# Kernel tuning notes

Hardware: AMD Instinct MI355X
Metric: run time of the kernel (lower is better)

Reference implementation:

```python
import jax, jax.numpy as jnp
import numpy as np

B, S, EMBED, HEADS = 2, 2048, 2048, 16
HEAD_DIM = EMBED // HEADS  # 128


def setup_inputs() -> dict:
    key = jax.random.key(0)
    k1, k2, k3 = jax.random.split(key, 3)
    x = jax.random.normal(k1, (B, S, EMBED), dtype=jnp.float32)
    # qkv_proj: Linear(EMBED -> 3*EMBED, bias=False); stored as [in, out]
    w_qkv = jax.random.normal(k2, (EMBED, 3 * EMBED), dtype=jnp.float32) / np.float32(np.sqrt(EMBED))
    # out_proj: Linear(EMBED -> EMBED, bias=False)
    w_out = jax.random.normal(k3, (EMBED, EMBED), dtype=jnp.float32) / np.float32(np.sqrt(EMBED))
    return {"x": x, "w_qkv": w_qkv, "w_out": w_out}


def reference(x, w_qkv, w_out):
    b, s, e = x.shape
    h, d = HEADS, e // HEADS
    qkv = x @ w_qkv                                  # [b, s, 3e]
    q, k, v = jnp.split(qkv, 3, axis=-1)             # each [b, s, e]
    q = q.reshape(b, s, h, d).transpose(0, 2, 1, 3)  # [b, h, s, d]
    k = k.reshape(b, s, h, d).transpose(0, 2, 1, 3)
    v = v.reshape(b, s, h, d).transpose(0, 2, 1, 3)
    scale = jnp.asarray(1.0 / np.sqrt(d), dtype=q.dtype)
    scores = jnp.einsum('bhqd,bhkd->bhqk', q, k) * scale  # [b, h, s, s]
    causal = jnp.tril(jnp.ones((s, s), dtype=bool))
    scores = jnp.where(causal, scores, -jnp.inf)
    attn = jax.nn.softmax(scores, axis=-1)
    ctx = jnp.einsum('bhqk,bhkd->bhqd', attn, v)     # [b, h, s, d]
    ctx = ctx.transpose(0, 2, 1, 3).reshape(b, s, e)
    return ctx @ w_out
```

## Files before the change

kernel.cpp:

```cpp
#include <hip/hip_runtime.h>
#include <cstdint>

#define S_LEN 2048
#define EMB   2048
#define NHEAD 16
#define HDIM  128
#define MROWS 4096
#define NQKV  6144

typedef __bf16 bf16x8 __attribute__((ext_vector_type(8)));
typedef __bf16 bf16x4 __attribute__((ext_vector_type(4)));
typedef float  f32x4  __attribute__((ext_vector_type(4)));

#define MFMA16(a, b, c) __builtin_amdgcn_mfma_f32_16x16x32_bf16((a), (b), (c), 0, 0, 0)

__device__ __forceinline__ unsigned short f2bf(float f) {
  unsigned u = __builtin_bit_cast(unsigned, f);
  u += 0x7fffu + ((u >> 16) & 1u);
  return (unsigned short)(u >> 16);
}
__device__ __forceinline__ float bf2f(unsigned short u) {
  unsigned v = ((unsigned)u) << 16;
  return __builtin_bit_cast(float, v);
}

__device__ __forceinline__ void gl_lds16(const unsigned short* g, unsigned short* l) {
  __builtin_amdgcn_global_load_lds(
      (const __attribute__((address_space(1))) void*)(uintptr_t)g,
      (__attribute__((address_space(3))) void*)(unsigned int)(uintptr_t)l,
      16, 0, 0);
}

__global__ void cast_bf16(const float* __restrict__ in, unsigned short* __restrict__ out, int n) {
  int i = (blockIdx.x * 256 + threadIdx.x) * 4;
  if (i >= n) return;
  float4 v = *(const float4*)(in + i);
  ushort4 o;
  o.x = f2bf(v.x); o.y = f2bf(v.y); o.z = f2bf(v.z); o.w = f2bf(v.w);
  *(ushort4*)(out + i) = o;
}

__global__ void transpose_cast(const float* __restrict__ in, unsigned short* __restrict__ out,
                               int R, int C) {
  __shared__ float tile[32][33];
  int bx = blockIdx.x << 5;
  int by = blockIdx.y << 5;
  int tx = threadIdx.x, ty = threadIdx.y;
  for (int j = 0; j < 32; j += 8)
    tile[ty + j][tx] = in[(size_t)(by + ty + j) * C + bx + tx];
  __syncthreads();
  for (int j = 0; j < 32; j += 8)
    out[(size_t)(bx + ty + j) * R + by + tx] = f2bf(tile[tx][ty + j]);
}

__global__ __launch_bounds__(256, 3) void gemm_qkv(const unsigned short* __restrict__ A,
                                                   const unsigned short* __restrict__ Bt,
                                                   unsigned short* __restrict__ Qo,
                                                   unsigned short* __restrict__ Ko,
                                                   unsigned short* __restrict__ Vt) {
  __shared__ __align__(16) unsigned short As[128 * 64];
  __shared__ __align__(16) unsigned short Bs[128 * 64];
  const int tid = threadIdx.x;
  const int n0 = blockIdx.x << 7;
  const int m0 = blockIdx.y << 7;
  const int wave = tid >> 6, lane = tid & 63;
  const int wm = (wave & 1) << 6, wn = (wave >> 1) << 6;
  const int fr = lane & 15, g = lane >> 4;
  const int q = tid >> 3;
  const int jp = tid & 7;
  f32x4 acc[4][4] = {};
  for (int k0 = 0; k0 < 2048; k0 += 64) {
    for (int i = 0; i < 4; ++i) {
      const int row = q + (i << 5);
      const int jsw = (jp ^ (row & 7)) << 3;
      gl_lds16(A + (size_t)(m0 + row) * 2048 + k0 + jsw, As + (row << 6) + (jp << 3));
      gl_lds16(Bt + (size_t)(n0 + row) * 2048 + k0 + jsw, Bs + (row << 6) + (jp << 3));
    }
    __builtin_amdgcn_s_waitcnt(0);
    __syncthreads();
    for (int ks = 0; ks < 2; ++ks) {
      const int slot = (((ks << 2) + g) ^ (fr & 7)) << 3;
      bf16x8 af[4], bfv[4];
      for (int i = 0; i < 4; ++i) af[i]  = *(const bf16x8*)(As + ((wm + (i << 4) + fr) << 6) + slot);
      for (int j = 0; j < 4; ++j) bfv[j] = *(const bf16x8*)(Bs + ((wn + (j << 4) + fr) << 6) + slot);
      for (int i = 0; i < 4; ++i)
        for (int j = 0; j < 4; ++j)
          acc[i][j] = MFMA16(af[i], bfv[j], acc[i][j]);
    }
    __syncthreads();
  }
  const int which = n0 >> 11;
  const int h = (n0 >> 7) & 15;
  const int bb = m0 >> 11;
  const int bh = bb * NHEAD + h;
  for (int i = 0; i < 4; ++i) {
    const int sl = (m0 & (S_LEN - 1)) + wm + (i << 4) + (g << 2);
    for (int j = 0; j < 4; ++j) {
      const int d = wn + (j << 4) + fr;
      if (which == 2) {
        ushort4 pk;
        pk.x = f2bf(acc[i][j][0]); pk.y = f2bf(acc[i][j][1]);
        pk.z = f2bf(acc[i][j][2]); pk.w = f2bf(acc[i][j][3]);
        *(ushort4*)(Vt + ((size_t)bh * HDIM + d) * S_LEN + sl) = pk;
      } else {
        unsigned short* dst = (which == 0) ? Qo : Ko;
        for (int r = 0; r < 4; ++r)
          dst[((size_t)bh * S_LEN + sl + r) * HDIM + d] = f2bf(acc[i][j][r]);
      }
    }
  }
}

__global__ __launch_bounds__(256, 3) void attn(const unsigned short* __restrict__ Qg,
                                               const unsigned short* __restrict__ Kg,
                                               const unsigned short* __restrict__ Vtg,
                                               unsigned short* __restrict__ ctx,
                                               unsigned short* __restrict__ Opart,
                                               float* __restrict__ Lp) {
  __shared__ __align__(16) unsigned short SA[16384];
  __shared__ __align__(16) unsigned short Ps[8192];
  unsigned short* Qs = SA;
  unsigned short* Ks = SA;
  unsigned short* Vs = SA + 8192;

  const int blk = blockIdx.x;
  const int bh = blk & 31;
  const int t = blk >> 5;
  int qt, kt0, nkt, part;
  if (t < 8)       { qt = t;     kt0 = 0;  nkt = 2 * t + 2;       part = -1; }
  else if (t < 16) { qt = t;     kt0 = 0;  nkt = 16;              part = (bh << 3) + (qt - 8); }
  else             { qt = t - 8; kt0 = 16; nkt = 2 * qt - 14;     part = 256 + (bh << 3) + (qt - 8); }

  const int tid = threadIdx.x, wave = tid >> 6, lane = tid & 63;
  const int fr = lane & 15, g = lane >> 4;

  const unsigned short* qsrc = Qg + ((size_t)bh * S_LEN + (qt << 7)) * HDIM;
  for (int i = 0; i < 8; ++i) {
    int s0 = (i * 256 + tid) << 3;
    int q = s0 >> 7, jp = (s0 >> 3) & 15;
    gl_lds16(qsrc + (q << 7) + ((jp ^ (q & 15)) << 3), Qs + s0);
  }
  __builtin_amdgcn_s_waitcnt(0);
  __syncthreads();

  bf16x8 qf[2][4];
  for (int nbq = 0; nbq < 2; ++nbq)
    for (int kd = 0; kd < 4; ++kd) {
      int q = (wave << 5) + (nbq << 4) + fr;
      qf[nbq][kd] = *(const bf16x8*)(Qs + (q << 7) + ((((kd << 2) + g) ^ fr) << 3));
    }
  __syncthreads();

  float lsum[2] = {0.f, 0.f};
  f32x4 oacc[2][8] = {};
  const float scale = 0.08838834764831845f;

  const unsigned short* kbase = Kg + (size_t)bh * S_LEN * HDIM;
  const unsigned short* vbase = Vtg + (size_t)bh * HDIM * S_LEN;

  for (int kti = 0; kti < nkt; ++kti) {
    const int kt = kt0 + kti;
    const unsigned short* ks = kbase + ((size_t)kt << 6) * HDIM;
    const unsigned short* vs = vbase + (kt << 6);
    for (int i = 0; i < 4; ++i) {
      int s0 = (i * 256 + tid) << 3;
      int key = s0 >> 7, jk = (s0 >> 3) & 15;
      gl_lds16(ks + (key << 7) + ((jk ^ (key & 15)) << 3), Ks + s0);
      int d = s0 >> 6, jv = (s0 >> 3) & 7;
      gl_lds16(vs + (size_t)d * S_LEN + ((jv ^ (d & 7)) << 3), Vs + s0);
    }
    __builtin_amdgcn_s_waitcnt(0);
    __syncthreads();

    f32x4 sacc[2][4] = {};
    for (int kd = 0; kd < 4; ++kd)
      for (int kb = 0; kb < 4; ++kb) {
        bf16x8 kf = *(const bf16x8*)(Ks + (((kb << 4) + fr) << 7) + ((((kd << 2) + g) ^ fr) << 3));
        sacc[0][kb] = MFMA16(kf, qf[0][kd], sacc[0][kb]);
        sacc[1][kb] = MFMA16(kf, qf[1][kd], sacc[1][kb]);
      }

    const bool diag = (kt >= 2 * qt);
    for (int nbq = 0; nbq < 2; ++nbq) {
      const int qg = (qt << 7) + (wave << 5) + (nbq << 4) + fr;
      float sum = 0.f;
      for (int kb = 0; kb < 4; ++kb) {
        float p[4];
        for (int r = 0; r < 4; ++r) {
          float v = sacc[nbq][kb][r] * scale;
          if (diag) {
            int keyg = (kt << 6) + (kb << 4) + (g << 2) + r;
            if (keyg > qg) v = -__builtin_inff();
          }
          p[r] = __expf(v);
          sum += p[r];
        }
        ushort4 pk;
        pk.x = f2bf(p[0]); pk.y = f2bf(p[1]); pk.z = f2bf(p[2]); pk.w = f2bf(p[3]);
        *(ushort4*)(Ps + (((wave << 3) + (nbq << 2) + kb) << 8) + (lane << 2)) = pk;
      }
      lsum[nbq] += sum;
    }

    __builtin_amdgcn_s_waitcnt(0);

    for (int kc = 0; kc < 2; ++kc) {
      const int kbr = (kc << 1) + (g >> 1);
      bf16x8 ap[2];
      for (int h2 = 0; h2 < 2; ++h2) {
        const unsigned short* pb =
            Ps + (((wave << 3) + (h2 << 2) + kbr) << 8) + ((g & 1) << 7) + (fr << 2);
        bf16x4 a0 = *(const bf16x4*)pb;
        bf16x4 a1 = *(const bf16x4*)(pb + 64);
        bf16x8 a;
        a[0] = a0[0]; a[1] = a0[1]; a[2] = a0[2]; a[3] = a0[3];
        a[4] = a1[0]; a[5] = a1[1]; a[6] = a1[2]; a[7] = a1[3];
        ap[h2] = a;
      }
      for (int nd = 0; nd < 8; ++nd) {
        bf16x8 bv = *(const bf16x8*)(Vs + (((nd << 4) + fr) << 6) + ((((kc << 2) + g) ^ (fr & 7)) << 3));
        oacc[0][nd] = MFMA16(ap[0], bv, oacc[0][nd]);
        oacc[1][nd] = MFMA16(ap[1], bv, oacc[1][nd]);
      }
    }
    __syncthreads();
  }

  for (int nbq = 0; nbq < 2; ++nbq) {
    lsum[nbq] += __shfl_xor(lsum[nbq], 16);
    lsum[nbq] += __shfl_xor(lsum[nbq], 32);
  }

  if (part < 0) {
    const int b = bh >> 4, h = bh & 15;
    for (int mq = 0; mq < 2; ++mq)
      for (int r = 0; r < 4; ++r) {
        float lv = __shfl(lsum[mq], (lane & 48) | ((g << 2) + r));
        const float il = 1.0f / lv;
        const int s = (qt << 7) + (wave << 5) + (mq << 4) + (g << 2) + r;
        unsigned short* dst = ctx + ((size_t)(b * S_LEN + s) * EMB) + (h << 7);
        for (int nd = 0; nd < 8; ++nd)
          dst[(nd << 4) + fr] = f2bf(oacc[mq][nd][r] * il);
      }
  } else {
    unsigned short* Ob = Opart + ((size_t)part << 14);
    for (int mq = 0; mq < 2; ++mq)
      for (int r = 0; r < 4; ++r) {
        const int ql = (wave << 5) + (mq << 4) + (g << 2) + r;
        unsigned short* dst = Ob + (ql << 7);
        for (int nd = 0; nd < 8; ++nd)
          dst[(nd << 4) + fr] = f2bf(oacc[mq][nd][r]);
      }
    if (g == 0)
      for (int nbq = 0; nbq < 2; ++nbq) {
        const int ql = (wave << 5) + (nbq << 4) + fr;
        Lp[(part << 7) + ql] = lsum[nbq];
      }
  }
}

__global__ void attn_combine(const unsigned short* __restrict__ Op,
                             const float* __restrict__ Lp,
                             unsigned short* __restrict__ ctx) {
  const int tid = threadIdx.x;
  const int rid = blockIdx.x * 16 + (tid >> 4);
  const int l16 = tid & 15;
  const int bh = rid >> 10;
  const int qtl = (rid >> 7) & 7;
  const int ql = rid & 127;
  const int p = (bh << 3) + qtl;
  const float lA = Lp[(p << 7) + ql];
  const float lB = Lp[((256 + p) << 7) + ql];
  const float il = 1.0f / (lA + lB);
  const int d0 = l16 << 3;
  const unsigned short* a = Op + ((size_t)p << 14) + (ql << 7) + d0;
  const unsigned short* b = Op + ((size_t)(256 + p) << 14) + (ql << 7) + d0;
  const int bb = bh >> 4, h = bh & 15;
  const int s = ((qtl + 8) << 7) + ql;
  unsigned short* dst = ctx + ((size_t)(bb * S_LEN + s) * EMB) + (h << 7) + d0;
  ushort4 va0 = *(const ushort4*)a, va1 = *(const ushort4*)(a + 4);
  ushort4 vb0 = *(const ushort4*)b, vb1 = *(const ushort4*)(b + 4);
  ushort4 o0, o1;
  o0.x = f2bf((bf2f(va0.x) + bf2f(vb0.x)) * il);
  o0.y = f2bf((bf2f(va0.y) + bf2f(vb0.y)) * il);
  o0.z = f2bf((bf2f(va0.z) + bf2f(vb0.z)) * il);
  o0.w = f2bf((bf2f(va0.w) + bf2f(vb0.w)) * il);
  o1.x = f2bf((bf2f(va1.x) + bf2f(vb1.x)) * il);
  o1.y = f2bf((bf2f(va1.y) + bf2f(vb1.y)) * il);
  o1.z = f2bf((bf2f(va1.z) + bf2f(vb1.z)) * il);
  o1.w = f2bf((bf2f(va1.w) + bf2f(vb1.w)) * il);
  *(ushort4*)dst = o0;
  *(ushort4*)(dst + 4) = o1;
}

__global__ __launch_bounds__(256, 3) void gemm_out(const unsigned short* __restrict__ A,
                                                   const unsigned short* __restrict__ Bt,
                                                   float* __restrict__ C) {
  __shared__ __align__(16) unsigned short As[128 * 64];
  __shared__ __align__(16) unsigned short Bs[128 * 64];
  const int tid = threadIdx.x;
  const int n0 = blockIdx.x << 7;
  const int m0 = blockIdx.y << 7;
  const int wave = tid >> 6, lane = tid & 63;
  const int wm = (wave & 1) << 6, wn = (wave >> 1) << 6;
  const int fr = lane & 15, g = lane >> 4;
  const int q = tid >> 3;
  const int jp = tid & 7;
  f32x4 acc[4][4] = {};
  for (int k0 = 0; k0 < 2048; k0 += 64) {
    for (int i = 0; i < 4; ++i) {
      const int row = q + (i << 5);
      const int jsw = (jp ^ (row & 7)) << 3;
      gl_lds16(A + (size_t)(m0 + row) * 2048 + k0 + jsw, As + (row << 6) + (jp << 3));
      gl_lds16(Bt + (size_t)(n0 + row) * 2048 + k0 + jsw, Bs + (row << 6) + (jp << 3));
    }
    __builtin_amdgcn_s_waitcnt(0);
    __syncthreads();
    for (int ks = 0; ks < 2; ++ks) {
      const int slot = (((ks << 2) + g) ^ (fr & 7)) << 3;
      bf16x8 af[4], bfv[4];
      for (int i = 0; i < 4; ++i) af[i]  = *(const bf16x8*)(As + ((wm + (i << 4) + fr) << 6) + slot);
      for (int j = 0; j < 4; ++j) bfv[j] = *(const bf16x8*)(Bs + ((wn + (j << 4) + fr) << 6) + slot);
      for (int i = 0; i < 4; ++i)
        for (int j = 0; j < 4; ++j)
          acc[i][j] = MFMA16(af[i], bfv[j], acc[i][j]);
    }
    __syncthreads();
  }
  for (int i = 0; i < 4; ++i) {
    const int row = m0 + wm + (i << 4) + (g << 2);
    for (int j = 0; j < 4; ++j) {
      const int col = n0 + wn + (j << 4) + fr;
      for (int r = 0; r < 4; ++r)
        C[(size_t)(row + r) * EMB + col] = acc[i][j][r];
    }
  }
}

extern "C" void kernel_launch(void* const* d_in, const int* in_sizes, int n_in,
                              void* d_out, int out_size, void* d_ws, size_t ws_size,
                              hipStream_t stream) {
  const float* x    = (const float*)d_in[0];
  const float* wqkv = (const float*)d_in[1];
  const float* wout = (const float*)d_in[2];
  float* out = (float*)d_out;

  unsigned short* ws = (unsigned short*)d_ws;
  const size_t NELEM = (size_t)MROWS * EMB;
  unsigned short* xb    = ws;
  unsigned short* wqkvT = xb + NELEM;
  unsigned short* woutT = wqkvT + (size_t)NQKV * EMB;
  unsigned short* Q     = woutT + (size_t)EMB * EMB;
  unsigned short* K     = Q + NELEM;
  unsigned short* Vt    = K + NELEM;
  unsigned short* ctx   = xb;
  unsigned short* Opart = wqkvT;
  float* Lp = (float*)(Opart + ((size_t)512 << 14));

  cast_bf16<<<8192, 256, 0, stream>>>(x, xb, (int)NELEM);
  transpose_cast<<<dim3(NQKV / 32, EMB / 32), dim3(32, 8), 0, stream>>>(wqkv, wqkvT, EMB, NQKV);
  transpose_cast<<<dim3(EMB / 32, EMB / 32), dim3(32, 8), 0, stream>>>(wout, woutT, EMB, EMB);
  gemm_qkv<<<dim3(NQKV / 128, MROWS / 128), 256, 0, stream>>>(xb, wqkvT, Q, K, Vt);
  attn<<<768, 256, 0, stream>>>(Q, K, Vt, ctx, Opart, Lp);
  attn_combine<<<2048, 256, 0, stream>>>(Opart, Lp, ctx);
  gemm_out<<<dim3(EMB / 128, MROWS / 128), 256, 0, stream>>>(ctx, woutT, out);
}
```

Baseline: 364.6 us.

## Replace QKV and output GEMMs with double-buffered 256x128-tile 8-wave pipeline

Both projection GEMMs now share a pipelined mainloop: 512-thread blocks compute 256x128 tiles and keep two K-stage buffers in dynamic LDS. The next stage's global-to-LDS loads are issued before the current stage's MFMAs, with a partial vmcnt wait so memory latency overlaps compute. The loop also splits the B fragment loads into two halves, raises wave priority around the MFMA bursts, and uses an XCD-aware block-index swizzle. The cost is 96KB of LDS per block, which limits occupancy to one block per CU, plus extra barriers per K step.

```diff
diff --git a/kernel.cpp b/kernel.cpp
--- a/kernel.cpp
+++ b/kernel.cpp
@@ -53,42 +53,115 @@
     out[(size_t)(bx + ty + j) * R + by + tx] = f2bf(tile[tx][ty + j]);
 }
 
-__global__ __launch_bounds__(256, 3) void gemm_qkv(const unsigned short* __restrict__ A,
-                                                   const unsigned short* __restrict__ Bt,
-                                                   unsigned short* __restrict__ Qo,
-                                                   unsigned short* __restrict__ Ko,
-                                                   unsigned short* __restrict__ Vt) {
-  __shared__ __align__(16) unsigned short As[128 * 64];
-  __shared__ __align__(16) unsigned short Bs[128 * 64];
+__device__ __forceinline__ void gemm_pipe(const unsigned short* __restrict__ Ap,
+                                          const unsigned short* __restrict__ Bp,
+                                          int m0, int n0, f32x4 (&acc)[4][4]) {
+  extern __shared__ unsigned short lds[];
+  unsigned short* As = lds;
+  unsigned short* Bs = lds + 32768;
   const int tid = threadIdx.x;
-  const int n0 = blockIdx.x << 7;
-  const int m0 = blockIdx.y << 7;
-  const int wave = tid >> 6, lane = tid & 63;
-  const int wm = (wave & 1) << 6, wn = (wave >> 1) << 6;
+  const int w = tid >> 6, lane = tid & 63;
   const int fr = lane & 15, g = lane >> 4;
-  const int q = tid >> 3;
-  const int jp = tid & 7;
+  const int wm = (w >> 1) << 6;
+  const int wn = (w & 1) << 6;
+  const int q = tid >> 3, jp = tid & 7;
+
+  auto stageA = [&](int buf, int kk) {
+#pragma unroll
+    for (int i = 0; i < 4; ++i) {
+      const int row = q + (i << 6);
+      gl_lds16(Ap + (size_t)(m0 + row) * 2048 + kk + ((jp ^ (row & 7)) << 3),
+               As + buf * 16384 + (row << 6) + (jp << 3));
+    }
+  };
+  auto stageB = [&](int buf, int kk) {
+#pragma unroll
+    for (int i = 0; i < 2; ++i) {
+      const int row = q + (i << 6);
+      gl_lds16(Bp + (size_t)(n0 + row) * 2048 + kk + ((jp ^ (row & 7)) << 3),
+               Bs + buf * 8192 + (row << 6) + (jp << 3));
+    }
+  };
+
+  stageA(0, 0); stageB(0, 0);
+  int cur = 0;
+#pragma unroll 2
+  for (int t = 0; t < 32; ++t) {
+    if (t < 31) {
+      const int kn = (t + 1) << 6;
+      stageA(cur ^ 1, kn); stageB(cur ^ 1, kn);
+      asm volatile("s_waitcnt vmcnt(6)" ::: "memory");
+    } else {
+      asm volatile("s_waitcnt vmcnt(0)" ::: "memory");
+    }
+    __builtin_amdgcn_s_barrier();
+    asm volatile("" ::: "memory");
+
+    const unsigned short* Ab = As + cur * 16384;
+    const unsigned short* Bb = Bs + cur * 8192;
+
+    bf16x8 af[4][2], bv[2][2];
+#pragma unroll
+    for (int i = 0; i < 4; ++i)
+#pragma unroll
+      for (int ks = 0; ks < 2; ++ks)
+        af[i][ks] = *(const bf16x8*)(Ab + ((wm + (i << 4) + fr) << 6) +
+                                     ((((ks << 2) + g) ^ (fr & 7)) << 3));
+#pragma unroll
+    for (int j = 0; j < 2; ++j)
+#pragma unroll
+      for (int ks = 0; ks < 2; ++ks)
+        bv[j][ks] = *(const bf16x8*)(Bb + ((wn + (j << 4) + fr) << 6) +
+                                     ((((ks << 2) + g) ^ (fr & 7)) << 3));
+    __builtin_amdgcn_s_setprio(1);
+#pragma unroll
+    for (int ks = 0; ks < 2; ++ks)
+#pragma unroll
+      for (int i = 0; i < 4; ++i)
+#pragma unroll
+        for (int j = 0; j < 2; ++j)
+          acc[i][j] = MFMA16(af[i][ks], bv[j][ks], acc[i][j]);
+    __builtin_amdgcn_s_setprio(0);
+    asm volatile("" ::: "memory");
+    __builtin_amdgcn_s_barrier();
+
+    bf16x8 bw[2][2];
+#pragma unroll
+    for (int j = 0; j < 2; ++j)
+#pragma unroll
+      for (int ks = 0; ks < 2; ++ks)
+        bw[j][ks] = *(const bf16x8*)(Bb + ((wn + ((j + 2) << 4) + fr) << 6) +
+                                     ((((ks << 2) + g) ^ (fr & 7)) << 3));
+    __builtin_amdgcn_s_setprio(1);
+#pragma unroll
+    for (int ks = 0; ks < 2; ++ks)
+#pragma unroll
+      for (int i = 0; i < 4; ++i)
+#pragma unroll
+        for (int j = 0; j < 2; ++j)
+          acc[i][j + 2] = MFMA16(af[i][ks], bw[j][ks], acc[i][j + 2]);
+    __builtin_amdgcn_s_setprio(0);
+    asm volatile("" ::: "memory");
+    __builtin_amdgcn_s_barrier();
+    cur ^= 1;
+  }
+}
+
+__global__ __launch_bounds__(512, 2) void gemm8_qkv(const unsigned short* __restrict__ A,
+                                                    const unsigned short* __restrict__ Bt,
+                                                    unsigned short* __restrict__ Qo,
+                                                    unsigned short* __restrict__ Ko,
+                                                    unsigned short* __restrict__ Vt) {
+  const int bid = blockIdx.x;
+  const int wg = (bid & 7) * 96 + (bid >> 3);
+  const int mt = wg / 48, nt = wg - mt * 48;
+  const int m0 = mt << 8, n0 = nt << 7;
   f32x4 acc[4][4] = {};
-  for (int k0 = 0; k0 < 2048; k0 += 64) {
-    for (int i = 0; i < 4; ++i) {
-      const int row = q + (i << 5);
-      const int jsw = (jp ^ (row & 7)) << 3;
-      gl_lds16(A + (size_t)(m0 + row) * 2048 + k0 + jsw, As + (row << 6) + (jp << 3));
-      gl_lds16(Bt + (size_t)(n0 + row) * 2048 + k0 + jsw, Bs + (row << 6) + (jp << 3));
-    }
-    __builtin_amdgcn_s_waitcnt(0);
-    __syncthreads();
-    for (int ks = 0; ks < 2; ++ks) {
-      const int slot = (((ks << 2) + g) ^ (fr & 7)) << 3;
-      bf16x8 af[4], bfv[4];
-      for (int i = 0; i < 4; ++i) af[i]  = *(const bf16x8*)(As + ((wm + (i << 4) + fr) << 6) + slot);
-      for (int j = 0; j < 4; ++j) bfv[j] = *(const bf16x8*)(Bs + ((wn + (j << 4) + fr) << 6) + slot);
-      for (int i = 0; i < 4; ++i)
-        for (int j = 0; j < 4; ++j)
-          acc[i][j] = MFMA16(af[i], bfv[j], acc[i][j]);
-    }
-    __syncthreads();
-  }
+  gemm_pipe(A, Bt, m0, n0, acc);
+
+  const int tid = threadIdx.x, w = tid >> 6, lane = tid & 63;
+  const int fr = lane & 15, g = lane >> 4;
+  const int wm = (w >> 1) << 6, wn = (w & 1) << 6;
   const int which = n0 >> 11;
   const int h = (n0 >> 7) & 15;
   const int bb = m0 >> 11;
@@ -107,6 +180,29 @@
         for (int r = 0; r < 4; ++r)
           dst[((size_t)bh * S_LEN + sl + r) * HDIM + d] = f2bf(acc[i][j][r]);
       }
+    }
+  }
+}
+
+__global__ __launch_bounds__(512, 2) void gemm8_out(const unsigned short* __restrict__ A,
+                                                    const unsigned short* __restrict__ Bt,
+                                                    float* __restrict__ C) {
+  const int bid = blockIdx.x;
+  const int wg = (bid & 7) * 32 + (bid >> 3);
+  const int mt = wg >> 4, nt = wg & 15;
+  const int m0 = mt << 8, n0 = nt << 7;
+  f32x4 acc[4][4] = {};
+  gemm_pipe(A, Bt, m0, n0, acc);
+
+  const int tid = threadIdx.x, w = tid >> 6, lane = tid & 63;
+  const int fr = lane & 15, g = lane >> 4;
+  const int wm = (w >> 1) << 6, wn = (w & 1) << 6;
+  for (int i = 0; i < 4; ++i) {
+    const int row = m0 + wm + (i << 4) + (g << 2);
+    for (int j = 0; j < 4; ++j) {
+      const int col = n0 + wn + (j << 4) + fr;
+      for (int r = 0; r < 4; ++r)
+        C[(size_t)(row + r) * EMB + col] = acc[i][j][r];
     }
   }
 }
@@ -293,50 +389,6 @@
   *(ushort4*)(dst + 4) = o1;
 }
 
-__global__ __launch_bounds__(256, 3) void gemm_out(const unsigned short* __restrict__ A,
-                                                   const unsigned short* __restrict__ Bt,
-                                                   float* __restrict__ C) {
-  __shared__ __align__(16) unsigned short As[128 * 64];
-  __shared__ __align__(16) unsigned short Bs[128 * 64];
-  const int tid = threadIdx.x;
-  const int n0 = blockIdx.x << 7;
-  const int m0 = blockIdx.y << 7;
-  const int wave = tid >> 6, lane = tid & 63;
-  const int wm = (wave & 1) << 6, wn = (wave >> 1) << 6;
-  const int fr = lane & 15, g = lane >> 4;
-  const int q = tid >> 3;
-  const int jp = tid & 7;
-  f32x4 acc[4][4] = {};
-  for (int k0 = 0; k0 < 2048; k0 += 64) {
-    for (int i = 0; i < 4; ++i) {
-      const int row = q + (i << 5);
-      const int jsw = (jp ^ (row & 7)) << 3;
-      gl_lds16(A + (size_t)(m0 + row) * 2048 + k0 + jsw, As + (row << 6) + (jp << 3));
-      gl_lds16(Bt + (size_t)(n0 + row) * 2048 + k0 + jsw, Bs + (row << 6) + (jp << 3));
-    }
-    __builtin_amdgcn_s_waitcnt(0);
-    __syncthreads();
-    for (int ks = 0; ks < 2; ++ks) {
-      const int slot = (((ks << 2) + g) ^ (fr & 7)) << 3;
-      bf16x8 af[4], bfv[4];
-      for (int i = 0; i < 4; ++i) af[i]  = *(const bf16x8*)(As + ((wm + (i << 4) + fr) << 6) + slot);
-      for (int j = 0; j < 4; ++j) bfv[j] = *(const bf16x8*)(Bs + ((wn + (j << 4) + fr) << 6) + slot);
-      for (int i = 0; i < 4; ++i)
-        for (int j = 0; j < 4; ++j)
-          acc[i][j] = MFMA16(af[i], bfv[j], acc[i][j]);
-    }
-    __syncthreads();
-  }
-  for (int i = 0; i < 4; ++i) {
-    const int row = m0 + wm + (i << 4) + (g << 2);
-    for (int j = 0; j < 4; ++j) {
-      const int col = n0 + wn + (j << 4) + fr;
-      for (int r = 0; r < 4; ++r)
-        C[(size_t)(row + r) * EMB + col] = acc[i][j][r];
-    }
-  }
-}
-
 extern "C" void kernel_launch(void* const* d_in, const int* in_sizes, int n_in,
                               void* d_out, int out_size, void* d_ws, size_t ws_size,
                               hipStream_t stream) {
@@ -357,11 +409,20 @@
   unsigned short* Opart = wqkvT;
   float* Lp = (float*)(Opart + ((size_t)512 << 14));
 
+  static bool attr_done = false;
+  if (!attr_done) {
+    (void)hipFuncSetAttribute((const void*)gemm8_qkv,
+                              hipFuncAttributeMaxDynamicSharedMemorySize, 98304);
+    (void)hipFuncSetAttribute((const void*)gemm8_out,
+                              hipFuncAttributeMaxDynamicSharedMemorySize, 98304);
+    attr_done = true;
+  }
+
   cast_bf16<<<8192, 256, 0, stream>>>(x, xb, (int)NELEM);
   transpose_cast<<<dim3(NQKV / 32, EMB / 32), dim3(32, 8), 0, stream>>>(wqkv, wqkvT, EMB, NQKV);
   transpose_cast<<<dim3(EMB / 32, EMB / 32), dim3(32, 8), 0, stream>>>(wout, woutT, EMB, EMB);
-  gemm_qkv<<<dim3(NQKV / 128, MROWS / 128), 256, 0, stream>>>(xb, wqkvT, Q, K, Vt);
+  gemm8_qkv<<<768, 512, 98304, stream>>>(xb, wqkvT, Q, K, Vt);
   attn<<<768, 256, 0, stream>>>(Q, K, Vt, ctx, Opart, Lp);
   attn_combine<<<2048, 256, 0, stream>>>(Opart, Lp, ctx);
-  gemm_out<<<dim3(EMB / 128, MROWS / 128), 256, 0, stream>>>(ctx, woutT, out);
-}
+  gemm8_out<<<256, 512, 98304, stream>>>(ctx, woutT, out);
+}
```

New measurement: 364.6 us. About the same (-0.0%).

## Rewrite QKV GEMM as 256x192 double-buffered 8-wave kernel with staged loads

Applied to the files above, without the earlier changes.

Replaces the 128x128 single-buffered QKV projection GEMM with a 512-thread kernel that computes 256x192 tiles. It double-buffers A and B in dynamic LDS and splits each k-step into three barrier-separated phases, so the next tile's global-to-LDS loads overlap MFMA work. It also uses s_setprio around the MFMA bursts and remaps block IDs to group neighbouring tiles. The aim is to hide memory latency and raise data reuse per block. In exchange it needs 112KB of LDS and more registers, which limits occupancy, and the hand-tuned vmcnt waits are fragile.

```diff
diff --git a/kernel.cpp b/kernel.cpp
--- a/kernel.cpp
+++ b/kernel.cpp
@@ -53,59 +53,147 @@
     out[(size_t)(bx + ty + j) * R + by + tx] = f2bf(tile[tx][ty + j]);
 }
 
-__global__ __launch_bounds__(256, 3) void gemm_qkv(const unsigned short* __restrict__ A,
-                                                   const unsigned short* __restrict__ Bt,
-                                                   unsigned short* __restrict__ Qo,
-                                                   unsigned short* __restrict__ Ko,
-                                                   unsigned short* __restrict__ Vt) {
-  __shared__ __align__(16) unsigned short As[128 * 64];
-  __shared__ __align__(16) unsigned short Bs[128 * 64];
-  const int tid = threadIdx.x;
-  const int n0 = blockIdx.x << 7;
-  const int m0 = blockIdx.y << 7;
-  const int wave = tid >> 6, lane = tid & 63;
-  const int wm = (wave & 1) << 6, wn = (wave >> 1) << 6;
+__global__ __launch_bounds__(512, 2) void gemm_qkv8(const unsigned short* __restrict__ A,
+                                                    const unsigned short* __restrict__ Bt,
+                                                    unsigned short* __restrict__ Qo,
+                                                    unsigned short* __restrict__ Ko,
+                                                    unsigned short* __restrict__ Vt) {
+  extern __shared__ unsigned short lds[];
+  unsigned short* Abuf = lds;
+  unsigned short* Bbuf = lds + 32768;
+
+  const int tid = threadIdx.x, w = tid >> 6, lane = tid & 63;
   const int fr = lane & 15, g = lane >> 4;
-  const int q = tid >> 3;
-  const int jp = tid & 7;
-  f32x4 acc[4][4] = {};
-  for (int k0 = 0; k0 < 2048; k0 += 64) {
-    for (int i = 0; i < 4; ++i) {
-      const int row = q + (i << 5);
-      const int jsw = (jp ^ (row & 7)) << 3;
-      gl_lds16(A + (size_t)(m0 + row) * 2048 + k0 + jsw, As + (row << 6) + (jp << 3));
-      gl_lds16(Bt + (size_t)(n0 + row) * 2048 + k0 + jsw, Bs + (row << 6) + (jp << 3));
-    }
-    __builtin_amdgcn_s_waitcnt(0);
-    __syncthreads();
-    for (int ks = 0; ks < 2; ++ks) {
-      const int slot = (((ks << 2) + g) ^ (fr & 7)) << 3;
-      bf16x8 af[4], bfv[4];
-      for (int i = 0; i < 4; ++i) af[i]  = *(const bf16x8*)(As + ((wm + (i << 4) + fr) << 6) + slot);
-      for (int j = 0; j < 4; ++j) bfv[j] = *(const bf16x8*)(Bs + ((wn + (j << 4) + fr) << 6) + slot);
-      for (int i = 0; i < 4; ++i)
-        for (int j = 0; j < 4; ++j)
-          acc[i][j] = MFMA16(af[i], bfv[j], acc[i][j]);
-    }
-    __syncthreads();
-  }
-  const int which = n0 >> 11;
-  const int h = (n0 >> 7) & 15;
-  const int bb = m0 >> 11;
-  const int bh = bb * NHEAD + h;
-  for (int i = 0; i < 4; ++i) {
-    const int sl = (m0 & (S_LEN - 1)) + wm + (i << 4) + (g << 2);
-    for (int j = 0; j < 4; ++j) {
-      const int d = wn + (j << 4) + fr;
+  const int gm = w >> 2, gn = w & 3;
+  const int srow = tid >> 3, jp = tid & 7;
+
+  const int bid = blockIdx.x;
+  const int wg = (bid & 7) * 64 + (bid >> 3);
+  const int mt = wg >> 5, nt = wg & 31;
+  const int m0 = mt << 8;
+  const int n0 = nt * 192;
+
+  auto issueB = [&](int buf, int kk, int third) {
+    const int row = (third << 6) + srow;
+    gl_lds16(Bt + (size_t)(n0 + row) * 2048 + kk + ((jp ^ (row & 7)) << 3),
+             Bbuf + buf * 12288 + (row << 6) + (jp << 3));
+  };
+  auto issueA = [&](int buf, int kk, int q) {
+    const int row = (q << 6) + srow;
+    gl_lds16(A + (size_t)(m0 + row) * 2048 + kk + ((jp ^ (row & 7)) << 3),
+             Abuf + buf * 16384 + (row << 6) + (jp << 3));
+  };
+
+  f32x4 acc[8][3] = {};
+  bf16x8 alo[4][2], ahi[4][2], bv[2][2], bc2[2];
+
+  issueB(0, 0, 0); issueB(0, 0, 1); issueB(0, 0, 2);
+  issueA(0, 0, 0); issueA(0, 0, 1); issueA(0, 0, 2); issueA(0, 0, 3);
+
+  for (int t = 0; t < 32; ++t) {
+    const int cb = t & 1, nb = cb ^ 1;
+    const unsigned short* Ab = Abuf + cb * 16384;
+    const unsigned short* Bb = Bbuf + cb * 12288;
+    const int kn = (t + 1) << 6;
+
+    asm volatile("s_waitcnt vmcnt(2)" ::: "memory");
+    asm volatile("" ::: "memory");
+    __builtin_amdgcn_s_barrier();
+    asm volatile("" ::: "memory");
+    if (t < 31) { issueB(nb, kn, 0); issueB(nb, kn, 1); issueB(nb, kn, 2); }
+#pragma unroll
+    for (int r = 0; r < 4; ++r)
+#pragma unroll
+      for (int ks = 0; ks < 2; ++ks)
+        alo[r][ks] = *(const bf16x8*)(Ab + ((gm * 64 + r * 16 + fr) << 6) +
+                                      ((((ks << 2) + g) ^ (fr & 7)) << 3));
+#pragma unroll
+    for (int c = 0; c < 2; ++c)
+#pragma unroll
+      for (int ks = 0; ks < 2; ++ks)
+        bv[c][ks] = *(const bf16x8*)(Bb + ((gn * 48 + c * 16 + fr) << 6) +
+                                     ((((ks << 2) + g) ^ (fr & 7)) << 3));
+    __builtin_amdgcn_s_setprio(1);
+#pragma unroll
+    for (int ks = 0; ks < 2; ++ks)
+#pragma unroll
+      for (int r = 0; r < 4; ++r)
+#pragma unroll
+        for (int c = 0; c < 2; ++c)
+          acc[r][c] = MFMA16(alo[r][ks], bv[c][ks], acc[r][c]);
+    __builtin_amdgcn_s_setprio(0);
+
+    if (t < 31) { asm volatile("s_waitcnt vmcnt(3)" ::: "memory"); }
+    else        { asm volatile("s_waitcnt vmcnt(0)" ::: "memory"); }
+    asm volatile("" ::: "memory");
+    __builtin_amdgcn_s_barrier();
+    asm volatile("" ::: "memory");
+    if (t < 31) { issueA(nb, kn, 0); issueA(nb, kn, 1); }
+#pragma unroll
+    for (int ks = 0; ks < 2; ++ks)
+      bc2[ks] = *(const bf16x8*)(Bb + ((gn * 48 + 32 + fr) << 6) +
+                                 ((((ks << 2) + g) ^ (fr & 7)) << 3));
+    __builtin_amdgcn_s_setprio(1);
+#pragma unroll
+    for (int ks = 0; ks < 2; ++ks)
+#pragma unroll
+      for (int r = 0; r < 4; ++r)
+        acc[r][2] = MFMA16(alo[r][ks], bc2[ks], acc[r][2]);
+    __builtin_amdgcn_s_setprio(0);
+#pragma unroll
+    for (int r = 0; r < 4; ++r)
+#pragma unroll
+      for (int ks = 0; ks < 2; ++ks)
+        ahi[r][ks] = *(const bf16x8*)(Ab + ((128 + gm * 64 + r * 16 + fr) << 6) +
+                                      ((((ks << 2) + g) ^ (fr & 7)) << 3));
+    __builtin_amdgcn_s_setprio(1);
+#pragma unroll
+    for (int ks = 0; ks < 2; ++ks)
+#pragma unroll
+      for (int r = 0; r < 4; ++r)
+        acc[4 + r][2] = MFMA16(ahi[r][ks], bc2[ks], acc[4 + r][2]);
+    __builtin_amdgcn_s_setprio(0);
+
+    asm volatile("" ::: "memory");
+    __builtin_amdgcn_s_barrier();
+    asm volatile("" ::: "memory");
+    if (t < 31) { issueA(nb, kn, 2); issueA(nb, kn, 3); }
+#pragma unroll
+    for (int c = 0; c < 2; ++c)
+#pragma unroll
+      for (int ks = 0; ks < 2; ++ks)
+        bv[c][ks] = *(const bf16x8*)(Bb + ((gn * 48 + c * 16 + fr) << 6) +
+                                     ((((ks << 2) + g) ^ (fr & 7)) << 3));
+    __builtin_amdgcn_s_setprio(1);
+#pragma unroll
+    for (int ks = 0; ks < 2; ++ks)
+#pragma unroll
+      for (int r = 0; r < 4; ++r)
+#pragma unroll
+        for (int c = 0; c < 2; ++c)
+          acc[4 + r][c] = MFMA16(ahi[r][ks], bv[c][ks], acc[4 + r][c]);
+    __builtin_amdgcn_s_setprio(0);
+  }
+
+  const int rowb = m0 & (S_LEN - 1);
+  const int bbase = (m0 >> 11) * NHEAD;
+  for (int r = 0; r < 8; ++r) {
+    const int sl = rowb + ((r >> 2) << 7) + (gm << 6) + ((r & 3) << 4) + (g << 2);
+    for (int c = 0; c < 3; ++c) {
+      const int ncol = n0 + gn * 48 + c * 16;
+      const int which = ncol >> 11;
+      const int h = (ncol >> 7) & 15;
+      const int d = (ncol & 127) + fr;
+      const int bh = bbase + h;
       if (which == 2) {
         ushort4 pk;
-        pk.x = f2bf(acc[i][j][0]); pk.y = f2bf(acc[i][j][1]);
-        pk.z = f2bf(acc[i][j][2]); pk.w = f2bf(acc[i][j][3]);
+        pk.x = f2bf(acc[r][c][0]); pk.y = f2bf(acc[r][c][1]);
+        pk.z = f2bf(acc[r][c][2]); pk.w = f2bf(acc[r][c][3]);
         *(ushort4*)(Vt + ((size_t)bh * HDIM + d) * S_LEN + sl) = pk;
       } else {
-        unsigned short* dst = (which == 0) ? Qo : Ko;
-        for (int r = 0; r < 4; ++r)
-          dst[((size_t)bh * S_LEN + sl + r) * HDIM + d] = f2bf(acc[i][j][r]);
+        unsigned short* dst = which ? Ko : Qo;
+        for (int q4 = 0; q4 < 4; ++q4)
+          dst[((size_t)bh * S_LEN + sl + q4) * HDIM + d] = f2bf(acc[r][c][q4]);
       }
     }
   }
@@ -196,7 +284,8 @@
           sum += p[r];
         }
         ushort4 pk;
-        pk.x = f2bf(p[0]); pk.y = f2bf(p[1]); pk.z = f2bf(p[2]); pk.w = f2bf(p[3]);
+        pk.x = f2bf(p[0]); pk.y = f2bf(p[1]);
+        pk.z = f2bf(p[2]); pk.w = f2bf(p[3]);
         *(ushort4*)(Ps + (((wave << 3) + (nbq << 2) + kb) << 8) + (lane << 2)) = pk;
       }
       lsum[nbq] += sum;
@@ -357,10 +446,17 @@
   unsigned short* Opart = wqkvT;
   float* Lp = (float*)(Opart + ((size_t)512 << 14));
 
+  static bool attr_done = false;
+  if (!attr_done) {
+    (void)hipFuncSetAttribute((const void*)gemm_qkv8,
+                              hipFuncAttributeMaxDynamicSharedMemorySize, 114688);
+    attr_done = true;
+  }
+
   cast_bf16<<<8192, 256, 0, stream>>>(x, xb, (int)NELEM);
   transpose_cast<<<dim3(NQKV / 32, EMB / 32), dim3(32, 8), 0, stream>>>(wqkv, wqkvT, EMB, NQKV);
   transpose_cast<<<dim3(EMB / 32, EMB / 32), dim3(32, 8), 0, stream>>>(wout, woutT, EMB, EMB);
-  gemm_qkv<<<dim3(NQKV / 128, MROWS / 128), 256, 0, stream>>>(xb, wqkvT, Q, K, Vt);
+  gemm_qkv8<<<512, 512, 114688, stream>>>(xb, wqkvT, Q, K, Vt);
   attn<<<768, 256, 0, stream>>>(Q, K, Vt, ctx, Opart, Lp);
   attn_combine<<<2048, 256, 0, stream>>>(Opart, Lp, ctx);
   gemm_out<<<dim3(EMB / 128, MROWS / 128), 256, 0, stream>>>(ctx, woutT, out);
```

New measurement: 365.1 us. About the same (+0.1%).
